# Optimization experiments

Measured on AMD Instinct MI355X. Metric: run time of the kernel, lower is better.

The kernel has to match this reference:

```python
import jax, jax.numpy as jnp
import numpy as np

N_GAUSSIANS = 512
N_PIXELS = 262144  # 512x512 image


def setup_inputs() -> dict:
    key = jax.random.key(0)
    k1, k2, k3, k4, k5 = jax.random.split(key, 5)
    x = jax.random.uniform(k1, (N_PIXELS, 2), dtype=jnp.float32)
    alphas = (1.0 / N_GAUSSIANS) ** 0.5 * jax.random.uniform(k2, (N_GAUSSIANS, 1), dtype=jnp.float32)
    means = jax.random.uniform(k3, (N_GAUSSIANS, 2), dtype=jnp.float32)
    rotations = jnp.pi * jax.random.uniform(k4, (N_GAUSSIANS, 1), dtype=jnp.float32)
    scales = 0.1 * jax.random.uniform(k5, (N_GAUSSIANS, 2), dtype=jnp.float32)
    return {"x": x, "alphas": alphas, "means": means, "rotations": rotations, "scales": scales}


def _inv2x2(m):
    # m: [N, 2, 2] -> elementwise 2x2 inverse
    a, b = m[:, 0, 0], m[:, 0, 1]
    c, d = m[:, 1, 0], m[:, 1, 1]
    det = a * d - b * c
    inv = jnp.stack([jnp.stack([d, -b], axis=-1),
                     jnp.stack([-c, a], axis=-1)], axis=-2)
    return inv / det[:, None, None]


def reference(x, alphas, means, rotations, scales):
    rot = rotations[:, 0]                       # [N]
    cth, sth = jnp.cos(rot), jnp.sin(rot)
    s0, s1 = scales[:, 0], scales[:, 1]
    # RS = R @ diag(s): [N, 2, 2]
    RS = jnp.stack([s0 * cth, -s1 * sth, s0 * sth, s1 * cth], axis=-1).reshape(-1, 2, 2)
    RSSR = jnp.einsum('nij,nkj->nik', RS, RS)   # RS @ RS^T
    cov = _inv2x2(RSSR)                          # [N, 2, 2]
    rel = x[:, None, :] - means[None, :, :]      # [P, N, 2]
    q = jnp.einsum('pni,nij,pnj->pn', rel, cov, rel)  # quadratic form [P, N]
    g = jnp.exp(-q / 2)                          # [P, N]
    return g @ alphas                            # [P, 1]
```

## Files before the change

kernel.cpp:

```cpp
#include <hip/hip_runtime.h>

#define NG 512
#define NPX 262144
#define BLOCK 256
#define GTILE 8

#if __has_builtin(__builtin_amdgcn_exp2f)
  #define KSCALE 0.72134752044448170368f
  #define EXPNEG(w) __builtin_amdgcn_exp2f(-(w))
#else
  #define KSCALE 0.5f
  #define EXPNEG(w) __expf(-(w))
#endif

__global__ __launch_bounds__(BLOCK, 4)
void gsplat_kernel(const float* __restrict__ x,
                   const float* __restrict__ alphas,
                   const float* __restrict__ means,
                   const float* __restrict__ rotations,
                   const float* __restrict__ scales,
                   float* __restrict__ out)
{
    __shared__ float4 ga[NG];
    __shared__ float2 gb[NG];

    for (int n = threadIdx.x; n < NG; n += BLOCK) {
        float rot = rotations[n];
        float sth, cth;
        sincosf(rot, &sth, &cth);
        float s0 = scales[2 * n + 0];
        float s1 = scales[2 * n + 1];
        float r00 = s0 * cth, r01 = -s1 * sth;
        float r10 = s0 * sth, r11 =  s1 * cth;
        float Ar = r00 * r00 + r01 * r01;
        float Br = r00 * r10 + r01 * r11;
        float Dr = r10 * r10 + r11 * r11;
        float det = Ar * Dr - Br * Br;
        float kc00 =  KSCALE * Dr / det;
        float kc01 = -KSCALE * Br / det;
        float p00 = sqrtf(kc00);
        float p01 = kc01 / p00;
        float p11 = sqrtf(KSCALE / Dr);
        float mx = means[2 * n + 0];
        float my = means[2 * n + 1];
        float nuoff = -(p00 * mx + p01 * my);
        float nvoff = -(p11 * my);
        ga[n] = make_float4(p00, p01, nuoff, alphas[n]);
        gb[n] = make_float2(p11, nvoff);
    }
    __syncthreads();

    int tid = blockIdx.x * BLOCK + threadIdx.x;
    float2 xv = ((const float2*)x)[tid];
    float x0 = xv.x, y0 = xv.y;

    float acc0 = 0.0f, acc1 = 0.0f;
    for (int t = 0; t < NG; t += GTILE) {
        float4 a[GTILE];
        float2 b[GTILE];
        #pragma unroll
        for (int j = 0; j < GTILE; ++j) {
            a[j] = ga[t + j];
            b[j] = gb[t + j];
        }
        #pragma unroll
        for (int j = 0; j < GTILE; ++j) {
            float u = fmaf(a[j].x, x0, fmaf(a[j].y, y0, a[j].z));
            float v = fmaf(b[j].x, y0, b[j].y);
            float w = fmaf(v, v, u * u);
            float e = EXPNEG(w);
            if (j & 1) acc1 = fmaf(a[j].w, e, acc1);
            else       acc0 = fmaf(a[j].w, e, acc0);
        }
    }

    out[tid] = acc0 + acc1;
}

extern "C" void kernel_launch(void* const* d_in, const int* in_sizes, int n_in,
                              void* d_out, int out_size, void* d_ws, size_t ws_size,
                              hipStream_t stream) {
    const float* x         = (const float*)d_in[0];
    const float* alphas    = (const float*)d_in[1];
    const float* means     = (const float*)d_in[2];
    const float* rotations = (const float*)d_in[3];
    const float* scales    = (const float*)d_in[4];
    float* out = (float*)d_out;

    int grid = NPX / BLOCK;
    gsplat_kernel<<<grid, BLOCK, 0, stream>>>(x, alphas, means, rotations, scales, out);
}
```

Baseline: 91.84 us.

## Split gaussian prep into separate kernel and process two pixels per thread with packed math

Moves the per-gaussian covariance and Cholesky-style precompute into a separate prep kernel that writes coefficients to workspace, so the main kernel reads uniform coefficients from global memory instead of rebuilding them in shared memory in every block. Each thread now handles two pixels using 2-wide float vectors, which allows packed FP32 arithmetic. Alpha is folded into the exponent as log2(alpha), so the multiply-accumulate becomes a plain add. This adds a second kernel launch and relies on scalar or constant-cache loads of the coefficients. log2 of alpha also fails if an alpha is zero, giving -inf, which exp2 still maps to zero.

```diff
diff --git a/kernel.cpp b/kernel.cpp
--- a/kernel.cpp
+++ b/kernel.cpp
@@ -4,77 +4,82 @@
 #define NPX 262144
 #define BLOCK 256
 #define GTILE 8
+#define CPG 6
+
+typedef float v2f __attribute__((ext_vector_type(2)));
 
 #if __has_builtin(__builtin_amdgcn_exp2f)
   #define KSCALE 0.72134752044448170368f
-  #define EXPNEG(w) __builtin_amdgcn_exp2f(-(w))
+  #define EXP2F(w) __builtin_amdgcn_exp2f(w)
 #else
-  #define KSCALE 0.5f
-  #define EXPNEG(w) __expf(-(w))
+  #define KSCALE 0.72134752044448170368f
+  #define EXP2F(w) exp2f(w)
 #endif
 
-__global__ __launch_bounds__(BLOCK, 4)
+__global__ __launch_bounds__(256)
+void gsplat_prep(const float* __restrict__ alphas,
+                 const float* __restrict__ means,
+                 const float* __restrict__ rotations,
+                 const float* __restrict__ scales,
+                 float* __restrict__ cp)
+{
+    int n = blockIdx.x * 256 + threadIdx.x;
+    if (n >= NG) return;
+    float rot = rotations[n];
+    float sth, cth;
+    sincosf(rot, &sth, &cth);
+    float s0 = scales[2 * n + 0];
+    float s1 = scales[2 * n + 1];
+    float r00 = s0 * cth, r01 = -s1 * sth;
+    float r10 = s0 * sth, r11 =  s1 * cth;
+    float Ar = r00 * r00 + r01 * r01;
+    float Br = r00 * r10 + r01 * r11;
+    float Dr = r10 * r10 + r11 * r11;
+    float det = Ar * Dr - Br * Br;
+    float kc00 =  KSCALE * Dr / det;
+    float kc01 = -KSCALE * Br / det;
+    float p00 = sqrtf(kc00);
+    float p01 = kc01 / p00;
+    float p11 = sqrtf(KSCALE / Dr);
+    float mx = means[2 * n + 0];
+    float my = means[2 * n + 1];
+    cp[n * CPG + 0] = p00;
+    cp[n * CPG + 1] = p01;
+    cp[n * CPG + 2] = -(p00 * mx + p01 * my);
+    cp[n * CPG + 3] = p11;
+    cp[n * CPG + 4] = -(p11 * my);
+    cp[n * CPG + 5] = log2f(alphas[n]);
+}
+
+__global__ __launch_bounds__(BLOCK, 2)
 void gsplat_kernel(const float* __restrict__ x,
-                   const float* __restrict__ alphas,
-                   const float* __restrict__ means,
-                   const float* __restrict__ rotations,
-                   const float* __restrict__ scales,
+                   const float* __restrict__ cp,
                    float* __restrict__ out)
 {
-    __shared__ float4 ga[NG];
-    __shared__ float2 gb[NG];
+    int tid = blockIdx.x * BLOCK + threadIdx.x;
+    float4 xv = ((const float4*)x)[tid];
+    v2f X = { xv.x, xv.z };
+    v2f Y = { xv.y, xv.w };
 
-    for (int n = threadIdx.x; n < NG; n += BLOCK) {
-        float rot = rotations[n];
-        float sth, cth;
-        sincosf(rot, &sth, &cth);
-        float s0 = scales[2 * n + 0];
-        float s1 = scales[2 * n + 1];
-        float r00 = s0 * cth, r01 = -s1 * sth;
-        float r10 = s0 * sth, r11 =  s1 * cth;
-        float Ar = r00 * r00 + r01 * r01;
-        float Br = r00 * r10 + r01 * r11;
-        float Dr = r10 * r10 + r11 * r11;
-        float det = Ar * Dr - Br * Br;
-        float kc00 =  KSCALE * Dr / det;
-        float kc01 = -KSCALE * Br / det;
-        float p00 = sqrtf(kc00);
-        float p01 = kc01 / p00;
-        float p11 = sqrtf(KSCALE / Dr);
-        float mx = means[2 * n + 0];
-        float my = means[2 * n + 1];
-        float nuoff = -(p00 * mx + p01 * my);
-        float nvoff = -(p11 * my);
-        ga[n] = make_float4(p00, p01, nuoff, alphas[n]);
-        gb[n] = make_float2(p11, nvoff);
-    }
-    __syncthreads();
+    v2f acc = { 0.0f, 0.0f };
+    for (int t = 0; t < NG; t += GTILE) {
+        float c[GTILE * CPG];
+        #pragma unroll
+        for (int j = 0; j < GTILE * CPG; ++j)
+            c[j] = cp[t * CPG + j];
 
-    int tid = blockIdx.x * BLOCK + threadIdx.x;
-    float2 xv = ((const float2*)x)[tid];
-    float x0 = xv.x, y0 = xv.y;
-
-    float acc0 = 0.0f, acc1 = 0.0f;
-    for (int t = 0; t < NG; t += GTILE) {
-        float4 a[GTILE];
-        float2 b[GTILE];
         #pragma unroll
         for (int j = 0; j < GTILE; ++j) {
-            a[j] = ga[t + j];
-            b[j] = gb[t + j];
-        }
-        #pragma unroll
-        for (int j = 0; j < GTILE; ++j) {
-            float u = fmaf(a[j].x, x0, fmaf(a[j].y, y0, a[j].z));
-            float v = fmaf(b[j].x, y0, b[j].y);
-            float w = fmaf(v, v, u * u);
-            float e = EXPNEG(w);
-            if (j & 1) acc1 = fmaf(a[j].w, e, acc1);
-            else       acc0 = fmaf(a[j].w, e, acc0);
+            const float* g = &c[j * CPG];
+            v2f u = g[0] * X + g[1] * Y + g[2];
+            v2f v = g[3] * Y + g[4];
+            v2f w = g[5] - u * u - v * v;
+            v2f e = { EXP2F(w.x), EXP2F(w.y) };
+            acc += e;
         }
     }
 
-    out[tid] = acc0 + acc1;
+    ((float2*)out)[tid] = make_float2(acc.x, acc.y);
 }
 
 extern "C" void kernel_launch(void* const* d_in, const int* in_sizes, int n_in,
@@ -86,7 +91,9 @@
     const float* rotations = (const float*)d_in[3];
     const float* scales    = (const float*)d_in[4];
     float* out = (float*)d_out;
+    float* cp  = (float*)d_ws;
 
-    int grid = NPX / BLOCK;
-    gsplat_kernel<<<grid, BLOCK, 0, stream>>>(x, alphas, means, rotations, scales, out);
+    gsplat_prep<<<(NG + 255) / 256, 256, 0, stream>>>(alphas, means, rotations, scales, cp);
+    int grid = NPX / (BLOCK * 2);
+    gsplat_kernel<<<grid, BLOCK, 0, stream>>>(x, cp, out);
 }
```

After: 93.05 us. Within noise of the previous version (+1.3%).

## Bin pixels into spatial cells and cull distant Gaussians per cell

Applied to the files above, without the earlier changes.

Adds a binning pass that scatters pixels into a 32x32 grid of cells using atomics. The splat kernel then evaluates only those Gaussians whose bounding-box lower bound on the exponent exceeds a cutoff for each cell. It also folds alpha into the exponent as log2(alpha) and evaluates Gaussian pairs with 2-wide vector math, handling two pixels per thread. In exchange it adds a memset, an extra kernel, per-block Gaussian setup, scattered output writes, and a fixed per-cell capacity that would silently drop pixels if a cell overflows.

```diff
diff --git a/kernel.cpp b/kernel.cpp
--- a/kernel.cpp
+++ b/kernel.cpp
@@ -2,29 +2,70 @@
 
 #define NG 512
 #define NPX 262144
-#define BLOCK 256
-#define GTILE 8
+#define GRID1D 32
+#define NCELL (GRID1D * GRID1D)
+#define CELLCAP 512
+#define KSCALE 0.72134752044448170368f
+#define WCULL  -30.0f
 
-#if __has_builtin(__builtin_amdgcn_exp2f)
-  #define KSCALE 0.72134752044448170368f
-  #define EXPNEG(w) __builtin_amdgcn_exp2f(-(w))
-#else
-  #define KSCALE 0.5f
-  #define EXPNEG(w) __expf(-(w))
-#endif
+typedef float v2f __attribute__((ext_vector_type(2)));
 
-__global__ __launch_bounds__(BLOCK, 4)
-void gsplat_kernel(const float* __restrict__ x,
-                   const float* __restrict__ alphas,
-                   const float* __restrict__ means,
-                   const float* __restrict__ rotations,
-                   const float* __restrict__ scales,
-                   float* __restrict__ out)
+
+__global__ __launch_bounds__(256)
+void bin_kernel(const float* __restrict__ x, int* __restrict__ cur,
+                float2* __restrict__ sxy, int* __restrict__ sidx)
 {
-    __shared__ float4 ga[NG];
-    __shared__ float2 gb[NG];
+    int tid = blockIdx.x * 256 + threadIdx.x;
+    float2 p = ((const float2*)x)[tid];
+    int cx = min((int)(p.x * GRID1D), GRID1D - 1);
+    int cy = min((int)(p.y * GRID1D), GRID1D - 1);
+    int cell = cy * GRID1D + cx;
+    int pos = atomicAdd(&cur[cell], 1);
+    if (pos < CELLCAP) {
+        sxy[cell * CELLCAP + pos] = p;
+        sidx[cell * CELLCAP + pos] = tid;
+    }
+}
 
-    for (int n = threadIdx.x; n < NG; n += BLOCK) {
+struct GPair {
+    v2f p00, p01, nu, p11, nv, l2a;
+};
+
+__device__ inline v2f pair_term(const GPair& g, float X, float Y) {
+    v2f u = g.p00 * X + g.p01 * Y + g.nu;
+    v2f v = g.p11 * Y + g.nv;
+    v2f w = g.l2a - u * u - v * v;
+    v2f e;
+    e.x = __builtin_amdgcn_exp2f(w.x);
+    e.y = __builtin_amdgcn_exp2f(w.y);
+    return e;
+}
+
+__global__ __launch_bounds__(128, 4)
+void splat_kernel(const int* __restrict__ cur,
+                  const float2* __restrict__ sxy,
+                  const int* __restrict__ sidx,
+                  const float* __restrict__ alphas,
+                  const float* __restrict__ means,
+                  const float* __restrict__ rotations,
+                  const float* __restrict__ scales,
+                  float* __restrict__ out)
+{
+    __shared__ GPair gp[(NG / 2) + 8];
+    __shared__ int nkept;
+
+    int tid  = threadIdx.x;
+    int cell = blockIdx.x >> 1;
+    int sub  = blockIdx.x & 1;
+    int cx = cell & (GRID1D - 1);
+    int cy = cell >> 5;
+    float bx0 = cx * (1.0f / GRID1D), bx1 = bx0 + (1.0f / GRID1D);
+    float by0 = cy * (1.0f / GRID1D), by1 = by0 + (1.0f / GRID1D);
+
+    if (tid == 0) nkept = 0;
+    __syncthreads();
+
+    for (int n = tid; n < NG; n += 128) {
         float rot = rotations[n];
         float sth, cth;
         sincosf(rot, &sth, &cth);
@@ -43,38 +84,64 @@
         float p11 = sqrtf(KSCALE / Dr);
         float mx = means[2 * n + 0];
         float my = means[2 * n + 1];
-        float nuoff = -(p00 * mx + p01 * my);
-        float nvoff = -(p11 * my);
-        ga[n] = make_float4(p00, p01, nuoff, alphas[n]);
-        gb[n] = make_float2(p11, nvoff);
+        float nu = -(p00 * mx + p01 * my);
+        float nv = -(p11 * my);
+        float l2a = log2f(alphas[n]);
+
+        float py0 = p01 * by0, py1 = p01 * by1;
+        float umin = p00 * bx0 + fminf(py0, py1) + nu;
+        float umax = p00 * bx1 + fmaxf(py0, py1) + nu;
+        float vmin = p11 * by0 + nv;
+        float vmax = p11 * by1 + nv;
+        float du = (umin > 0.0f) ? umin : ((umax < 0.0f) ? umax : 0.0f);
+        float dv = (vmin > 0.0f) ? vmin : ((vmax < 0.0f) ? vmax : 0.0f);
+        float wmax = l2a - du * du - dv * dv;
+
+        if (wmax > WCULL) {
+            int slot = atomicAdd(&nkept, 1);
+            int pr = slot >> 1, h = slot & 1;
+            gp[pr].p00[h] = p00; gp[pr].p01[h] = p01; gp[pr].nu[h]  = nu;
+            gp[pr].p11[h] = p11; gp[pr].nv[h]  = nv;  gp[pr].l2a[h] = l2a;
+        }
     }
     __syncthreads();
 
-    int tid = blockIdx.x * BLOCK + threadIdx.x;
-    float2 xv = ((const float2*)x)[tid];
-    float x0 = xv.x, y0 = xv.y;
+    int nk = nkept;
+    int nround = (nk + 7) & ~7;
+    if (tid < nround - nk) {
+        int slot = nk + tid;
+        int pr = slot >> 1, h = slot & 1;
+        gp[pr].p00[h] = 0.0f; gp[pr].p01[h] = 0.0f; gp[pr].nu[h]  = 0.0f;
+        gp[pr].p11[h] = 0.0f; gp[pr].nv[h]  = 0.0f; gp[pr].l2a[h] = -10000.0f;
+    }
+    __syncthreads();
+    int npairs = nround >> 1;
 
-    float acc0 = 0.0f, acc1 = 0.0f;
-    for (int t = 0; t < NG; t += GTILE) {
-        float4 a[GTILE];
-        float2 b[GTILE];
-        #pragma unroll
-        for (int j = 0; j < GTILE; ++j) {
-            a[j] = ga[t + j];
-            b[j] = gb[t + j];
+    int count = min(cur[cell], CELLCAP);
+    const float4* pxy = (const float4*)(sxy + cell * CELLCAP);
+    const int*    idx = sidx + cell * CELLCAP;
+
+    for (int p0 = tid + sub * 128; 2 * p0 < count; p0 += 256) {
+        float4 pv = pxy[p0];
+        float xa = pv.x, ya = pv.y;
+        float xb = pv.z, yb = pv.w;
+        v2f accA = {0.0f, 0.0f}, accB = {0.0f, 0.0f};
+
+        for (int t = 0; t < npairs; t += 4) {
+            GPair g0 = gp[t + 0];
+            GPair g1 = gp[t + 1];
+            GPair g2 = gp[t + 2];
+            GPair g3 = gp[t + 3];
+            accA += pair_term(g0, xa, ya);  accB += pair_term(g0, xb, yb);
+            accA += pair_term(g1, xa, ya);  accB += pair_term(g1, xb, yb);
+            accA += pair_term(g2, xa, ya);  accB += pair_term(g2, xb, yb);
+            accA += pair_term(g3, xa, ya);  accB += pair_term(g3, xb, yb);
         }
-        #pragma unroll
-        for (int j = 0; j < GTILE; ++j) {
-            float u = fmaf(a[j].x, x0, fmaf(a[j].y, y0, a[j].z));
-            float v = fmaf(b[j].x, y0, b[j].y);
-            float w = fmaf(v, v, u * u);
-            float e = EXPNEG(w);
-            if (j & 1) acc1 = fmaf(a[j].w, e, acc1);
-            else       acc0 = fmaf(a[j].w, e, acc0);
-        }
+
+        out[idx[2 * p0]] = accA.x + accA.y;
+        if (2 * p0 + 1 < count)
+            out[idx[2 * p0 + 1]] = accB.x + accB.y;
     }
-
-    out[tid] = acc0 + acc1;
 }
 
 extern "C" void kernel_launch(void* const* d_in, const int* in_sizes, int n_in,
@@ -87,6 +154,13 @@
     const float* scales    = (const float*)d_in[4];
     float* out = (float*)d_out;
 
-    int grid = NPX / BLOCK;
-    gsplat_kernel<<<grid, BLOCK, 0, stream>>>(x, alphas, means, rotations, scales, out);
+    char* ws = (char*)d_ws;
+    int*    cur  = (int*)ws;
+    float2* sxy  = (float2*)(ws + 4096);
+    int*    sidx = (int*)(ws + 4096 + (size_t)NCELL * CELLCAP * sizeof(float2));
+
+    hipMemsetAsync(cur, 0, NCELL * sizeof(int), stream);
+    bin_kernel<<<NPX / 256, 256, 0, stream>>>(x, cur, sxy, sidx);
+    splat_kernel<<<NCELL * 2, 128, 0, stream>>>(cur, sxy, sidx,
+                                                alphas, means, rotations, scales, out);
 }
```

Measured after the change: 140.1 us. +52.5%, slower.
